# Kernel tuning notes

Hardware: AMD Instinct MI355X
Metric: run time of the kernel (lower is better)

## Reference

```python
import jax, jax.numpy as jnp
import numpy as np

N_E = 1024      # nconcepts (codebook size)
E_DIM = 64      # cdim (codebook vector dim)
BETA = 0.25
LEGACY = True


def setup_inputs() -> dict:
    key = jax.random.key(0)
    k1, k2, k3 = jax.random.split(key, 3)
    z_ = jax.random.normal(k1, (32, 256, 32, 32), jnp.float32)
    # 1x1 conv dis_modulator: 256 -> 64 channels (stored as [out, in])
    conv_w = jax.random.normal(k2, (64, 256), jnp.float32) / np.sqrt(256.0)
    conv_b = jnp.zeros((64,), jnp.float32)
    # embedding.weight.data.uniform_(-1/n_e, 1/n_e)
    emb = jax.random.uniform(k3, (N_E, E_DIM), jnp.float32, -1.0 / N_E, 1.0 / N_E)
    return {"z_": z_, "conv_w": conv_w, "conv_b": conv_b, "emb": emb}


def _forward(z_, conv_w, conv_b, emb):
    sg = jax.lax.stop_gradient
    # dis_modulator: 1x1 conv == per-pixel linear map  (B,Cin,H,W)->(B,Cout,H,W)
    z = jnp.einsum('bchw,oc->bohw', z_, conv_w) + conv_b[None, :, None, None]
    B = z.shape[0]
    # torch .view(-1, e_dim): row-major flatten of (B,C,H,W) into chunks of e_dim
    zf = z.reshape(-1, E_DIM)  # [B*C*H*W/e_dim, e_dim]

    # contrastive term: mean pairwise cosine similarity of codebook rows
    d1 = emb @ emb.T                                  # [n_e, n_e]
    norms = jnp.linalg.norm(emb, axis=1)              # [n_e]
    cosine = d1 / (norms[:, None] * norms[None, :])
    contrastive = jnp.mean(cosine)

    # squared L2 distances: ||z||^2 + ||e||^2 - 2 z.e
    d = (jnp.sum(zf * zf, axis=1, keepdims=True)
         + jnp.sum(emb * emb, axis=1)[None, :]
         - 2.0 * (zf @ emb.T))                        # [N, n_e]
    idx = jnp.argmin(d, axis=1)                       # [N]
    z_q = emb[idx].reshape(z.shape)

    if LEGACY:
        loss = jnp.mean((sg(z_q) - z) ** 2) + BETA * jnp.mean((z_q - sg(z)) ** 2)
    else:
        loss = BETA * jnp.mean((sg(z_q) - z) ** 2) + jnp.mean((z_q - sg(z)) ** 2)
    # hessian_penalty(G, z_, G_z=z): G is an affine 1x1 conv, so the central
    # second difference G(z+x) - 2G(z) + G(z-x) is identically zero -> penalty = 0.
    loss = loss + contrastive

    # straight-through estimator
    z_q_st = z + sg(z_q - z)

    # replicate source exactly: flat zeros(B*n_e) scattered at codebook indices
    sampled = jnp.zeros((B * N_E,), z.dtype).at[idx].set(1.0).reshape(B, N_E)
    min_idx = idx.reshape(B, -1)
    return z_q_st, loss, sampled, min_idx


def reference(z_, conv_w, conv_b, emb):
    z_q, loss, sampled, min_idx = _forward(z_, conv_w, conv_b, emb)
    return z_q, loss, sampled, min_idx
```

## Files before the change

kernel.cpp:

```cpp
#include <hip/hip_runtime.h>

#define BATCH   32
#define CIN     256
#define COUT    64
#define HW      1024
#define NE      1024
#define ED      64
#define NROW    32768
#define ZTOT    2097152

#define OFF_LOSS 2097152
#define OFF_SAMP 2097153
#define OFF_IDX  2129921

#define CXSTR 132
#define CWSTR 68
#define ZSTR  132
#define ESTR  132

__global__ __launch_bounds__(256, 2) void k_pre(const float* __restrict__ x,
                                                const float* __restrict__ w,
                                                const float* __restrict__ bias,
                                                float* __restrict__ z,
                                                const float* __restrict__ emb,
                                                float* __restrict__ out_samp,
                                                float* __restrict__ enorm,
                                                float* __restrict__ cpart,
                                                unsigned int* __restrict__ counter) {
    __shared__ float SH[64 * CXSTR + 64 * CWSTR];
    int bx = blockIdx.x;
    int t  = threadIdx.x;

    if (bx < 128) {
        if (bx == 0 && t == 0) *counter = 0u;
        out_samp[bx * 256 + t] = 0.0f;
        return;
    }
    if (bx < 144) {
        float* invl = SH;
        float* S    = SH + 64;
        int b2 = bx - 128;
        int i0 = b2 * 64;
        if (t < 64) {
            const float* e = emb + (size_t)(i0 + t) * ED;
            float r8[8];
            #pragma unroll
            for (int s = 0; s < 8; s++) { float xx = e[s]; r8[s] = xx * xx; }
            #pragma unroll
            for (int m = 1; m < 8; m++) {
                #pragma unroll
                for (int s = 0; s < 8; s++) { float xx = e[8 * m + s]; r8[s] += xx * xx; }
            }
            float en = ((r8[0] + r8[1]) + (r8[2] + r8[3])) + ((r8[4] + r8[5]) + (r8[6] + r8[7]));
            invl[t] = 1.0f / sqrtf(en);
        }
        __syncthreads();
        int d = t & 63, q = t >> 6;
        float s = 0.0f;
        #pragma unroll
        for (int m = 0; m < 16; m++) {
            int il = q + 4 * m;
            s = fmaf(emb[(size_t)(i0 + il) * ED + d], invl[il], s);
        }
        S[t] = s;
        __syncthreads();
        if (t < 64)
            cpart[b2 * 64 + t] = (S[t] + S[t + 64]) + (S[t + 128] + S[t + 192]);
        return;
    }
    if (bx < 148) {
        int j = (bx - 144) * 256 + t;
        const float* e = emb + (size_t)j * ED;
        float r8[8];
        #pragma unroll
        for (int s = 0; s < 8; s++) { float xx = e[s]; r8[s] = xx * xx; }
        #pragma unroll
        for (int m = 1; m < 8; m++) {
            #pragma unroll
            for (int s = 0; s < 8; s++) { float xx = e[8 * m + s]; r8[s] += xx * xx; }
        }
        enorm[j] = ((r8[0] + r8[1]) + (r8[2] + r8[3])) + ((r8[4] + r8[5]) + (r8[6] + r8[7]));
        return;
    }

    float* Xs = SH;
    float* Ws = SH + 64 * CXSTR;
    int cbx = bx - 148;
    int b   = cbx >> 3;
    int p0  = (cbx & 7) * 128;
    int pg  = t & 15;
    int og  = t >> 4;
    float acc[8][4];
    #pragma unroll
    for (int i = 0; i < 8; i++)
        #pragma unroll
        for (int j = 0; j < 4; j++) acc[i][j] = 0.0f;

    for (int c0 = 0; c0 < CIN; c0 += 64) {
        __syncthreads();
        {
            int u = t & 31, cc = t >> 5;
            #pragma unroll
            for (int m = 0; m < 8; m++) {
                int c = cc + 8 * m;
                float4 v = *(const float4*)&x[(size_t)(b * CIN + c0 + c) * HW + p0 + 4 * u];
                *(float4*)&Xs[c * CXSTR + 4 * u] = v;
            }
            int u2 = t & 15, o2 = t >> 4;
            #pragma unroll
            for (int m = 0; m < 4; m++) {
                int o = o2 + 16 * m;
                float4 v = *(const float4*)&w[o * CIN + c0 + 4 * u2];
                Ws[(4 * u2 + 0) * CWSTR + o] = v.x;
                Ws[(4 * u2 + 1) * CWSTR + o] = v.y;
                Ws[(4 * u2 + 2) * CWSTR + o] = v.z;
                Ws[(4 * u2 + 3) * CWSTR + o] = v.w;
            }
        }
        __syncthreads();
        #pragma unroll 4
        for (int k = 0; k < 64; k++) {
            float4 xa4 = *(const float4*)&Xs[k * CXSTR + 4 * pg];
            float4 xb4 = *(const float4*)&Xs[k * CXSTR + 64 + 4 * pg];
            float4 wv4 = *(const float4*)&Ws[k * CWSTR + 4 * og];
            float xa[8] = {xa4.x, xa4.y, xa4.z, xa4.w, xb4.x, xb4.y, xb4.z, xb4.w};
            float wb[4] = {wv4.x, wv4.y, wv4.z, wv4.w};
            #pragma unroll
            for (int i = 0; i < 8; i++)
                #pragma unroll
                for (int j = 0; j < 4; j++)
                    acc[i][j] = fmaf(xa[i], wb[j], acc[i][j]);
        }
    }
    #pragma unroll
    for (int j = 0; j < 4; j++) {
        int o = 4 * og + j;
        float bv = bias[o];
        float4 lo, hi;
        lo.x = acc[0][j] + bv; lo.y = acc[1][j] + bv;
        lo.z = acc[2][j] + bv; lo.w = acc[3][j] + bv;
        hi.x = acc[4][j] + bv; hi.y = acc[5][j] + bv;
        hi.z = acc[6][j] + bv; hi.w = acc[7][j] + bv;
        *(float4*)&z[(size_t)(b * COUT + o) * HW + p0 + 4 * pg]      = lo;
        *(float4*)&z[(size_t)(b * COUT + o) * HW + p0 + 64 + 4 * pg] = hi;
    }
}

__global__ __launch_bounds__(256, 2) void k_dist(const float* __restrict__ z,
                                                 const float* __restrict__ emb,
                                                 const float* __restrict__ enorm,
                                                 const float* __restrict__ cpart,
                                                 float* __restrict__ out_idx,
                                                 float* __restrict__ out_samp,
                                                 float* __restrict__ out_zq,
                                                 float* __restrict__ ssep,
                                                 float* __restrict__ out_loss,
                                                 unsigned int* __restrict__ counter) {
    __shared__ float zs[64 * ZSTR];
    __shared__ float es[64 * ESTR];
    __shared__ float zn_s[128];
    __shared__ float en_s[128];
    __shared__ float warr[4];
    __shared__ int   lastflag;
    __shared__ float CS;
    float* redd_s = es;
    int*   redj_s = (int*)(es + 2048);
    int*   bj_s   = (int*)(es + 4096);
    int t = threadIdx.x;
    int row0 = blockIdx.x * 128;
    int rg = t & 15;
    int cg = t >> 4;

    {
        int k = t & 63, wv = t >> 6;
        #pragma unroll
        for (int m = 0; m < 8; m++) {
            int v = wv + 4 * m;
            float4 val;
            val.x = z[(size_t)(row0 + 4 * v + 0) * ED + k];
            val.y = z[(size_t)(row0 + 4 * v + 1) * ED + k];
            val.z = z[(size_t)(row0 + 4 * v + 2) * ED + k];
            val.w = z[(size_t)(row0 + 4 * v + 3) * ED + k];
            *(float4*)&zs[k * ZSTR + 4 * v] = val;
        }
    }
    __syncthreads();
    if (t < 128) {
        float r8[8];
        #pragma unroll
        for (int s = 0; s < 8; s++) { float xx = zs[s * ZSTR + t]; r8[s] = xx * xx; }
        #pragma unroll
        for (int m = 1; m < 8; m++) {
            #pragma unroll
            for (int s = 0; s < 8; s++) { float xx = zs[(8 * m + s) * ZSTR + t]; r8[s] += xx * xx; }
        }
        zn_s[t] = ((r8[0] + r8[1]) + (r8[2] + r8[3])) + ((r8[4] + r8[5]) + (r8[6] + r8[7]));
    }

    float bestd[8];
    int   bestj[8];
    #pragma unroll
    for (int i = 0; i < 8; i++) { bestd[i] = __builtin_huge_valf(); bestj[i] = 0; }

    for (int ch = 0; ch < 8; ch++) {
        int c0 = ch * 128;
        __syncthreads();
        {
            int k = t & 63, wv = t >> 6;
            #pragma unroll
            for (int m = 0; m < 8; m++) {
                int v = wv + 4 * m;
                float4 val;
                val.x = emb[(size_t)(c0 + 4 * v + 0) * ED + k];
                val.y = emb[(size_t)(c0 + 4 * v + 1) * ED + k];
                val.z = emb[(size_t)(c0 + 4 * v + 2) * ED + k];
                val.w = emb[(size_t)(c0 + 4 * v + 3) * ED + k];
                *(float4*)&es[k * ESTR + 4 * v] = val;
            }
            if (t < 32) {
                float4 ev4 = *(const float4*)&enorm[c0 + 4 * t];
                *(float4*)&en_s[4 * t] = ev4;
            }
        }
        __syncthreads();

        float acc[8][8];
        #pragma unroll
        for (int i = 0; i < 8; i++)
            #pragma unroll
            for (int j = 0; j < 8; j++) acc[i][j] = 0.0f;

        #pragma unroll 4
        for (int k = 0; k < 64; k++) {
            float4 za = *(const float4*)&zs[k * ZSTR + 4 * rg];
            float4 zb = *(const float4*)&zs[k * ZSTR + 64 + 4 * rg];
            float4 e0 = *(const float4*)&es[k * ESTR + 8 * cg];
            float4 e1 = *(const float4*)&es[k * ESTR + 8 * cg + 4];
            float xa[8] = {za.x, za.y, za.z, za.w, zb.x, zb.y, zb.z, zb.w};
            float eb[8] = {e0.x, e0.y, e0.z, e0.w, e1.x, e1.y, e1.z, e1.w};
            #pragma unroll
            for (int i = 0; i < 8; i++)
                #pragma unroll
                for (int j = 0; j < 8; j++)
                    acc[i][j] = fmaf(xa[i], eb[j], acc[i][j]);
        }

        #pragma unroll
        for (int i = 0; i < 8; i++) {
            int rl = (i < 4) ? (4 * rg + i) : (64 + 4 * rg + (i - 4));
            float zn = zn_s[rl];
            #pragma unroll
            for (int j = 0; j < 8; j++) {
                int cl = 8 * cg + j;
                float A = zn + en_s[cl];
                float D = A - 2.0f * acc[i][j];
                if (D < bestd[i]) { bestd[i] = D; bestj[i] = c0 + cl; }
            }
        }
    }

    __syncthreads();
    #pragma unroll
    for (int i = 0; i < 8; i++) {
        int rl = (i < 4) ? (4 * rg + i) : (64 + 4 * rg + (i - 4));
        redd_s[cg * 128 + rl] = bestd[i];
        redj_s[cg * 128 + rl] = bestj[i];
    }
    __syncthreads();
    if (t < 128) {
        float bd = __builtin_huge_valf();
        int   bj = 0x7fffffff;
        #pragma unroll
        for (int c = 0; c < 16; c++) {
            float dd = redd_s[c * 128 + t];
            int   jj = redj_s[c * 128 + t];
            if (dd < bd || (dd == bd && jj < bj)) { bd = dd; bj = jj; }
        }
        int rowg = row0 + t;
        bj_s[t]       = bj;
        out_idx[rowg] = (float)bj;
        atomicExch(&out_samp[bj], 1.0f);
    }
    __syncthreads();

    {
        int r  = t & 127;
        int kq = t >> 7;
        int bj = bj_s[r];
        const float* er = emb + (size_t)bj * ED + kq * 32;
        float sq = 0.0f;
        #pragma unroll
        for (int m = 0; m < 8; m++) {
            float4 ev = *(const float4*)&er[4 * m];
            int kk = kq * 32 + 4 * m;
            float zv0 = zs[(kk + 0) * ZSTR + r];
            float zv1 = zs[(kk + 1) * ZSTR + r];
            float zv2 = zs[(kk + 2) * ZSTR + r];
            float zv3 = zs[(kk + 3) * ZSTR + r];
            float d0 = ev.x - zv0, d1 = ev.y - zv1, d2 = ev.z - zv2, d3 = ev.w - zv3;
            float4 o4;
            o4.x = zv0 + d0; o4.y = zv1 + d1; o4.z = zv2 + d2; o4.w = zv3 + d3;
            *(float4*)&out_zq[(size_t)(row0 + r) * ED + kk] = o4;
            sq += d0 * d0; sq += d1 * d1; sq += d2 * d2; sq += d3 * d3;
        }
        #pragma unroll
        for (int off = 32; off > 0; off >>= 1) sq += __shfl_down(sq, off, 64);
        if ((t & 63) == 0) warr[t >> 6] = sq;
    }
    __syncthreads();

    if (t == 0) {
        ssep[blockIdx.x] = (warr[0] + warr[1]) + (warr[2] + warr[3]);
        __threadfence();
        unsigned int old = atomicAdd(counter, 1u);
        lastflag = (old == 255u) ? 1 : 0;
    }
    __syncthreads();
    if (lastflag) {
        __threadfence();
        double* SD = (double*)es;
        const volatile float* sv = (const volatile float*)ssep;
        SD[t] = (double)sv[t];
        __syncthreads();
        #pragma unroll
        for (int off = 128; off > 0; off >>= 1) {
            if (t < off) SD[t] += SD[t + off];
            __syncthreads();
        }
        if (t < 64) {
            float v = 0.0f;
            #pragma unroll
            for (int m = 0; m < 16; m++) v += cpart[m * 64 + t];
            float sq = v * v;
            #pragma unroll
            for (int off = 32; off > 0; off >>= 1) sq += __shfl_down(sq, off, 64);
            if (t == 0) CS = sq / (1024.0f * 1024.0f);
        }
        __syncthreads();
        if (t == 0) {
            float m = (float)(SD[0] / (double)ZTOT);
            float loss = m + 0.25f * m;
            out_loss[0] = loss + CS;
        }
    }
}

extern "C" void kernel_launch(void* const* d_in, const int* in_sizes, int n_in,
                              void* d_out, int out_size, void* d_ws, size_t ws_size,
                              hipStream_t stream) {
    (void)in_sizes; (void)n_in; (void)out_size; (void)ws_size;
    const float* z_     = (const float*)d_in[0];
    const float* conv_w = (const float*)d_in[1];
    const float* conv_b = (const float*)d_in[2];
    const float* emb    = (const float*)d_in[3];

    float* out      = (float*)d_out;
    float* out_zq   = out;
    float* out_loss = out + OFF_LOSS;
    float* out_samp = out + OFF_SAMP;
    float* out_idx  = out + OFF_IDX;

    char*  ws       = (char*)d_ws;
    float* wz       = (float*)ws;
    float* enorm    = (float*)(ws + 8388608);
    float* cpart    = (float*)(ws + 8392704);
    float* ssep     = (float*)(ws + 8396800);
    unsigned int* counter = (unsigned int*)(ws + 8397824);

    k_pre  <<<404, 256, 0, stream>>>(z_, conv_w, conv_b, wz, emb, out_samp, enorm, cpart, counter);
    k_dist <<<256, 256, 0, stream>>>(wz, emb, enorm, cpart, out_idx, out_samp, out_zq, ssep, out_loss, counter);
}
```

Baseline: 183.9 us.

## Retile distance kernel to 64-row blocks with row-major smem and k-split codebook chunks

The distance/argmin kernel now handles 64 rows per block instead of 128 and launches 512 blocks, so more of the device's compute units get work. Shared memory switches from a k-major transposed layout to row-major padded rows loaded with float4 and coalesced global reads. Codebook chunks grow to 256 entries, staged in two 32-wide k halves, and each thread computes an 8x8 tile through float4 dot-product loads. This trades more codebook reloads per output row and a wider 32-way cross-thread reduction for better load coalescing and parallelism.

```diff
diff --git a/kernel.cpp b/kernel.cpp
--- a/kernel.cpp
+++ b/kernel.cpp
@@ -15,8 +15,8 @@
 
 #define CXSTR 132
 #define CWSTR 68
-#define ZSTR  132
-#define ESTR  132
+#define ZROWS 68
+#define EROWS 36
 
 __global__ __launch_bounds__(256, 2) void k_pre(const float* __restrict__ x,
                                                 const float* __restrict__ w,
@@ -156,10 +156,10 @@
                                                  float* __restrict__ ssep,
                                                  float* __restrict__ out_loss,
                                                  unsigned int* __restrict__ counter) {
-    __shared__ float zs[64 * ZSTR];
-    __shared__ float es[64 * ESTR];
-    __shared__ float zn_s[128];
-    __shared__ float en_s[128];
+    __shared__ float zs[64 * ZROWS];
+    __shared__ float es[256 * EROWS];
+    __shared__ float zn_s[64];
+    __shared__ float en_s[256];
     __shared__ float warr[4];
     __shared__ int   lastflag;
     __shared__ float CS;
@@ -167,32 +167,29 @@
     int*   redj_s = (int*)(es + 2048);
     int*   bj_s   = (int*)(es + 4096);
     int t = threadIdx.x;
-    int row0 = blockIdx.x * 128;
-    int rg = t & 15;
-    int cg = t >> 4;
+    int row0 = blockIdx.x * 64;
+    int rg = t >> 5;
+    int cg = t & 31;
 
     {
-        int k = t & 63, wv = t >> 6;
-        #pragma unroll
-        for (int m = 0; m < 8; m++) {
-            int v = wv + 4 * m;
-            float4 val;
-            val.x = z[(size_t)(row0 + 4 * v + 0) * ED + k];
-            val.y = z[(size_t)(row0 + 4 * v + 1) * ED + k];
-            val.z = z[(size_t)(row0 + 4 * v + 2) * ED + k];
-            val.w = z[(size_t)(row0 + 4 * v + 3) * ED + k];
-            *(float4*)&zs[k * ZSTR + 4 * v] = val;
-        }
-    }
-    __syncthreads();
-    if (t < 128) {
+        int k4 = t & 15, rr = t >> 4;
+        #pragma unroll
+        for (int m = 0; m < 4; m++) {
+            int r = rr + 16 * m;
+            float4 v = *(const float4*)&z[(size_t)(row0 + r) * ED + 4 * k4];
+            *(float4*)&zs[r * ZROWS + 4 * k4] = v;
+        }
+    }
+    __syncthreads();
+    if (t < 64) {
+        const float* zr = &zs[t * ZROWS];
         float r8[8];
         #pragma unroll
-        for (int s = 0; s < 8; s++) { float xx = zs[s * ZSTR + t]; r8[s] = xx * xx; }
+        for (int s = 0; s < 8; s++) { float xx = zr[s]; r8[s] = xx * xx; }
         #pragma unroll
         for (int m = 1; m < 8; m++) {
             #pragma unroll
-            for (int s = 0; s < 8; s++) { float xx = zs[(8 * m + s) * ZSTR + t]; r8[s] += xx * xx; }
+            for (int s = 0; s < 8; s++) { float xx = zr[8 * m + s]; r8[s] += xx * xx; }
         }
         zn_s[t] = ((r8[0] + r8[1]) + (r8[2] + r8[3])) + ((r8[4] + r8[5]) + (r8[6] + r8[7]));
     }
@@ -202,56 +199,59 @@
     #pragma unroll
     for (int i = 0; i < 8; i++) { bestd[i] = __builtin_huge_valf(); bestj[i] = 0; }
 
-    for (int ch = 0; ch < 8; ch++) {
-        int c0 = ch * 128;
-        __syncthreads();
-        {
-            int k = t & 63, wv = t >> 6;
-            #pragma unroll
-            for (int m = 0; m < 8; m++) {
-                int v = wv + 4 * m;
-                float4 val;
-                val.x = emb[(size_t)(c0 + 4 * v + 0) * ED + k];
-                val.y = emb[(size_t)(c0 + 4 * v + 1) * ED + k];
-                val.z = emb[(size_t)(c0 + 4 * v + 2) * ED + k];
-                val.w = emb[(size_t)(c0 + 4 * v + 3) * ED + k];
-                *(float4*)&es[k * ESTR + 4 * v] = val;
-            }
-            if (t < 32) {
-                float4 ev4 = *(const float4*)&enorm[c0 + 4 * t];
-                *(float4*)&en_s[4 * t] = ev4;
-            }
-        }
-        __syncthreads();
-
+    for (int ch = 0; ch < 4; ch++) {
+        int c0 = ch * 256;
         float acc[8][8];
         #pragma unroll
         for (int i = 0; i < 8; i++)
             #pragma unroll
             for (int j = 0; j < 8; j++) acc[i][j] = 0.0f;
 
-        #pragma unroll 4
-        for (int k = 0; k < 64; k++) {
-            float4 za = *(const float4*)&zs[k * ZSTR + 4 * rg];
-            float4 zb = *(const float4*)&zs[k * ZSTR + 64 + 4 * rg];
-            float4 e0 = *(const float4*)&es[k * ESTR + 8 * cg];
-            float4 e1 = *(const float4*)&es[k * ESTR + 8 * cg + 4];
-            float xa[8] = {za.x, za.y, za.z, za.w, zb.x, zb.y, zb.z, zb.w};
-            float eb[8] = {e0.x, e0.y, e0.z, e0.w, e1.x, e1.y, e1.z, e1.w};
-            #pragma unroll
-            for (int i = 0; i < 8; i++)
+        for (int kh = 0; kh < 2; kh++) {
+            __syncthreads();
+            {
+                int k4 = t & 7, cc = t >> 3;
+                #pragma unroll
+                for (int m = 0; m < 8; m++) {
+                    int c = cc + 32 * m;
+                    float4 v = *(const float4*)&emb[(size_t)(c0 + c) * ED + kh * 32 + 4 * k4];
+                    *(float4*)&es[c * EROWS + 4 * k4] = v;
+                }
+                if (kh == 0 && t < 64) {
+                    float4 ev = *(const float4*)&enorm[c0 + 4 * t];
+                    *(float4*)&en_s[4 * t] = ev;
+                }
+            }
+            __syncthreads();
+
+            int kb = kh * 32;
+            #pragma unroll 2
+            for (int ks = 0; ks < 8; ks++) {
+                float4 za[8], eb[8];
+                #pragma unroll
+                for (int i = 0; i < 8; i++)
+                    za[i] = *(const float4*)&zs[(rg + 8 * i) * ZROWS + kb + 4 * ks];
                 #pragma unroll
                 for (int j = 0; j < 8; j++)
-                    acc[i][j] = fmaf(xa[i], eb[j], acc[i][j]);
+                    eb[j] = *(const float4*)&es[(cg + 32 * j) * EROWS + 4 * ks];
+                #pragma unroll
+                for (int i = 0; i < 8; i++)
+                    #pragma unroll
+                    for (int j = 0; j < 8; j++) {
+                        acc[i][j] = fmaf(za[i].x, eb[j].x, acc[i][j]);
+                        acc[i][j] = fmaf(za[i].y, eb[j].y, acc[i][j]);
+                        acc[i][j] = fmaf(za[i].z, eb[j].z, acc[i][j]);
+                        acc[i][j] = fmaf(za[i].w, eb[j].w, acc[i][j]);
+                    }
+            }
         }
 
         #pragma unroll
         for (int i = 0; i < 8; i++) {
-            int rl = (i < 4) ? (4 * rg + i) : (64 + 4 * rg + (i - 4));
-            float zn = zn_s[rl];
+            float zn = zn_s[rg + 8 * i];
             #pragma unroll
             for (int j = 0; j < 8; j++) {
-                int cl = 8 * cg + j;
+                int cl = cg + 32 * j;
                 float A = zn + en_s[cl];
                 float D = A - 2.0f * acc[i][j];
                 if (D < bestd[i]) { bestd[i] = D; bestj[i] = c0 + cl; }
@@ -262,18 +262,18 @@
     __syncthreads();
     #pragma unroll
     for (int i = 0; i < 8; i++) {
-        int rl = (i < 4) ? (4 * rg + i) : (64 + 4 * rg + (i - 4));
-        redd_s[cg * 128 + rl] = bestd[i];
-        redj_s[cg * 128 + rl] = bestj[i];
-    }
-    __syncthreads();
-    if (t < 128) {
+        int rl = rg + 8 * i;
+        redd_s[cg * 64 + rl] = bestd[i];
+        redj_s[cg * 64 + rl] = bestj[i];
+    }
+    __syncthreads();
+    if (t < 64) {
         float bd = __builtin_huge_valf();
         int   bj = 0x7fffffff;
         #pragma unroll
-        for (int c = 0; c < 16; c++) {
-            float dd = redd_s[c * 128 + t];
-            int   jj = redj_s[c * 128 + t];
+        for (int c = 0; c < 32; c++) {
+            float dd = redd_s[c * 64 + t];
+            int   jj = redj_s[c * 64 + t];
             if (dd < bd || (dd == bd && jj < bj)) { bd = dd; bj = jj; }
         }
         int rowg = row0 + t;
@@ -284,23 +284,20 @@
     __syncthreads();
 
     {
-        int r  = t & 127;
-        int kq = t >> 7;
+        int r  = t & 63;
+        int kq = t >> 6;
         int bj = bj_s[r];
-        const float* er = emb + (size_t)bj * ED + kq * 32;
+        const float* er = emb + (size_t)bj * ED + kq * 16;
+        const float* zr = &zs[r * ZROWS + kq * 16];
         float sq = 0.0f;
         #pragma unroll
-        for (int m = 0; m < 8; m++) {
+        for (int m = 0; m < 4; m++) {
             float4 ev = *(const float4*)&er[4 * m];
-            int kk = kq * 32 + 4 * m;
-            float zv0 = zs[(kk + 0) * ZSTR + r];
-            float zv1 = zs[(kk + 1) * ZSTR + r];
-            float zv2 = zs[(kk + 2) * ZSTR + r];
-            float zv3 = zs[(kk + 3) * ZSTR + r];
-            float d0 = ev.x - zv0, d1 = ev.y - zv1, d2 = ev.z - zv2, d3 = ev.w - zv3;
+            float4 zv = *(const float4*)&zr[4 * m];
+            float d0 = ev.x - zv.x, d1 = ev.y - zv.y, d2 = ev.z - zv.z, d3 = ev.w - zv.w;
             float4 o4;
-            o4.x = zv0 + d0; o4.y = zv1 + d1; o4.z = zv2 + d2; o4.w = zv3 + d3;
-            *(float4*)&out_zq[(size_t)(row0 + r) * ED + kk] = o4;
+            o4.x = zv.x + d0; o4.y = zv.y + d1; o4.z = zv.z + d2; o4.w = zv.w + d3;
+            *(float4*)&out_zq[(size_t)(row0 + r) * ED + kq * 16 + 4 * m] = o4;
             sq += d0 * d0; sq += d1 * d1; sq += d2 * d2; sq += d3 * d3;
         }
         #pragma unroll
@@ -313,14 +310,14 @@
         ssep[blockIdx.x] = (warr[0] + warr[1]) + (warr[2] + warr[3]);
         __threadfence();
         unsigned int old = atomicAdd(counter, 1u);
-        lastflag = (old == 255u) ? 1 : 0;
+        lastflag = (old == 511u) ? 1 : 0;
     }
     __syncthreads();
     if (lastflag) {
         __threadfence();
         double* SD = (double*)es;
         const volatile float* sv = (const volatile float*)ssep;
-        SD[t] = (double)sv[t];
+        SD[t] = (double)sv[t] + (double)sv[t + 256];
         __syncthreads();
         #pragma unroll
         for (int off = 128; off > 0; off >>= 1) {
@@ -365,8 +362,8 @@
     float* enorm    = (float*)(ws + 8388608);
     float* cpart    = (float*)(ws + 8392704);
     float* ssep     = (float*)(ws + 8396800);
-    unsigned int* counter = (unsigned int*)(ws + 8397824);
+    unsigned int* counter = (unsigned int*)(ws + 8398848);
 
     k_pre  <<<404, 256, 0, stream>>>(z_, conv_w, conv_b, wz, emb, out_samp, enorm, cpart, counter);
-    k_dist <<<256, 256, 0, stream>>>(wz, emb, enorm, cpart, out_idx, out_samp, out_zq, ssep, out_loss, counter);
+    k_dist <<<512, 256, 0, stream>>>(wz, emb, enorm, cpart, out_idx, out_samp, out_zq, ssep, out_loss, counter);
 }
```

After: 185.3 us. About the same (+0.8%).

## Fuse 1x1 conv into distance kernel and keep z tile in shared memory

Applied to the files above, without the earlier changes.

The conv GEMM moves into the distance/argmin kernel, so each block computes its 64 flattened rows of z directly into shared memory. This removes the write of the 8 MB z intermediate to global memory and its read back. It relies on the fact that a 64-pixel strip of the conv output for one batch maps to 64 rows of the flattened view at stride 16. The tile shrinks from 128 to 64 rows and the grid grows to 512 blocks, which means more codebook reloads per row and smaller per-thread register tiles.

```diff
diff --git a/kernel.cpp b/kernel.cpp
--- a/kernel.cpp
+++ b/kernel.cpp
@@ -6,39 +6,32 @@
 #define HW      1024
 #define NE      1024
 #define ED      64
-#define NROW    32768
 #define ZTOT    2097152
 
 #define OFF_LOSS 2097152
 #define OFF_SAMP 2097153
 #define OFF_IDX  2129921
 
-#define CXSTR 132
-#define CWSTR 68
-#define ZSTR  132
-#define ESTR  132
-
-__global__ __launch_bounds__(256, 2) void k_pre(const float* __restrict__ x,
-                                                const float* __restrict__ w,
-                                                const float* __restrict__ bias,
-                                                float* __restrict__ z,
-                                                const float* __restrict__ emb,
-                                                float* __restrict__ out_samp,
-                                                float* __restrict__ enorm,
-                                                float* __restrict__ cpart,
-                                                unsigned int* __restrict__ counter) {
-    __shared__ float SH[64 * CXSTR + 64 * CWSTR];
+#define CSTR 66
+#define ESTR 132
+#define ZSTR 68
+
+__global__ __launch_bounds__(256) void k_con(const float* __restrict__ emb,
+                                             float* __restrict__ out_samp,
+                                             float* __restrict__ enorm,
+                                             float* __restrict__ cpart,
+                                             unsigned int* __restrict__ counter) {
+    __shared__ float SHc[320];
     int bx = blockIdx.x;
     int t  = threadIdx.x;
-
     if (bx < 128) {
         if (bx == 0 && t == 0) *counter = 0u;
         out_samp[bx * 256 + t] = 0.0f;
         return;
     }
     if (bx < 144) {
-        float* invl = SH;
-        float* S    = SH + 64;
+        float* invl = SHc;
+        float* S    = SHc + 64;
         int b2 = bx - 128;
         int i0 = b2 * 64;
         if (t < 64) {
@@ -68,7 +61,7 @@
             cpart[b2 * 64 + t] = (S[t] + S[t + 64]) + (S[t + 128] + S[t + 192]);
         return;
     }
-    if (bx < 148) {
+    {
         int j = (bx - 144) * 256 + t;
         const float* e = emb + (size_t)j * ED;
         float r8[8];
@@ -80,127 +73,116 @@
             for (int s = 0; s < 8; s++) { float xx = e[8 * m + s]; r8[s] += xx * xx; }
         }
         enorm[j] = ((r8[0] + r8[1]) + (r8[2] + r8[3])) + ((r8[4] + r8[5]) + (r8[6] + r8[7]));
-        return;
-    }
-
-    float* Xs = SH;
-    float* Ws = SH + 64 * CXSTR;
-    int cbx = bx - 148;
-    int b   = cbx >> 3;
-    int p0  = (cbx & 7) * 128;
-    int pg  = t & 15;
-    int og  = t >> 4;
-    float acc[8][4];
-    #pragma unroll
-    for (int i = 0; i < 8; i++)
-        #pragma unroll
-        for (int j = 0; j < 4; j++) acc[i][j] = 0.0f;
-
-    for (int c0 = 0; c0 < CIN; c0 += 64) {
-        __syncthreads();
-        {
-            int u = t & 31, cc = t >> 5;
-            #pragma unroll
-            for (int m = 0; m < 8; m++) {
-                int c = cc + 8 * m;
-                float4 v = *(const float4*)&x[(size_t)(b * CIN + c0 + c) * HW + p0 + 4 * u];
-                *(float4*)&Xs[c * CXSTR + 4 * u] = v;
-            }
-            int u2 = t & 15, o2 = t >> 4;
-            #pragma unroll
-            for (int m = 0; m < 4; m++) {
-                int o = o2 + 16 * m;
-                float4 v = *(const float4*)&w[o * CIN + c0 + 4 * u2];
-                Ws[(4 * u2 + 0) * CWSTR + o] = v.x;
-                Ws[(4 * u2 + 1) * CWSTR + o] = v.y;
-                Ws[(4 * u2 + 2) * CWSTR + o] = v.z;
-                Ws[(4 * u2 + 3) * CWSTR + o] = v.w;
-            }
-        }
-        __syncthreads();
-        #pragma unroll 4
-        for (int k = 0; k < 64; k++) {
-            float4 xa4 = *(const float4*)&Xs[k * CXSTR + 4 * pg];
-            float4 xb4 = *(const float4*)&Xs[k * CXSTR + 64 + 4 * pg];
-            float4 wv4 = *(const float4*)&Ws[k * CWSTR + 4 * og];
-            float xa[8] = {xa4.x, xa4.y, xa4.z, xa4.w, xb4.x, xb4.y, xb4.z, xb4.w};
-            float wb[4] = {wv4.x, wv4.y, wv4.z, wv4.w};
-            #pragma unroll
-            for (int i = 0; i < 8; i++)
-                #pragma unroll
-                for (int j = 0; j < 4; j++)
-                    acc[i][j] = fmaf(xa[i], wb[j], acc[i][j]);
-        }
-    }
-    #pragma unroll
-    for (int j = 0; j < 4; j++) {
-        int o = 4 * og + j;
-        float bv = bias[o];
-        float4 lo, hi;
-        lo.x = acc[0][j] + bv; lo.y = acc[1][j] + bv;
-        lo.z = acc[2][j] + bv; lo.w = acc[3][j] + bv;
-        hi.x = acc[4][j] + bv; hi.y = acc[5][j] + bv;
-        hi.z = acc[6][j] + bv; hi.w = acc[7][j] + bv;
-        *(float4*)&z[(size_t)(b * COUT + o) * HW + p0 + 4 * pg]      = lo;
-        *(float4*)&z[(size_t)(b * COUT + o) * HW + p0 + 64 + 4 * pg] = hi;
     }
 }
 
-__global__ __launch_bounds__(256, 2) void k_dist(const float* __restrict__ z,
-                                                 const float* __restrict__ emb,
-                                                 const float* __restrict__ enorm,
-                                                 const float* __restrict__ cpart,
-                                                 float* __restrict__ out_idx,
-                                                 float* __restrict__ out_samp,
-                                                 float* __restrict__ out_zq,
-                                                 float* __restrict__ ssep,
-                                                 float* __restrict__ out_loss,
-                                                 unsigned int* __restrict__ counter) {
+__global__ __launch_bounds__(256, 2) void k_fused(const float* __restrict__ x,
+                                                  const float* __restrict__ w,
+                                                  const float* __restrict__ bias,
+                                                  const float* __restrict__ emb,
+                                                  const float* __restrict__ enorm,
+                                                  const float* __restrict__ cpart,
+                                                  float* __restrict__ out_idx,
+                                                  float* __restrict__ out_samp,
+                                                  float* __restrict__ out_zq,
+                                                  float* __restrict__ ssep,
+                                                  float* __restrict__ out_loss,
+                                                  unsigned int* __restrict__ counter) {
+    __shared__ float SH[64 * CSTR * 2];
     __shared__ float zs[64 * ZSTR];
-    __shared__ float es[64 * ESTR];
-    __shared__ float zn_s[128];
+    __shared__ float zn_s[64];
     __shared__ float en_s[128];
     __shared__ float warr[4];
+    __shared__ int   bj_s[64];
     __shared__ int   lastflag;
     __shared__ float CS;
-    float* redd_s = es;
-    int*   redj_s = (int*)(es + 2048);
-    int*   bj_s   = (int*)(es + 4096);
-    int t = threadIdx.x;
-    int row0 = blockIdx.x * 128;
+    __shared__ double SD[256];
+    float* redd_s = SH;
+    int*   redj_s = (int*)(SH + 1024);
+
+    int t  = threadIdx.x;
+    int bx = blockIdx.x;
+    int b   = bx >> 4;
+    int p16 = bx & 15;
+    int p0  = p16 * 64;
+
+    {
+        float* Xs = SH;
+        float* Ws = SH + 64 * CSTR;
+        int pg = t & 15;
+        int og = t >> 4;
+        float acc[4][4];
+        #pragma unroll
+        for (int i = 0; i < 4; i++)
+            #pragma unroll
+            for (int j = 0; j < 4; j++) acc[i][j] = 0.0f;
+
+        for (int c0 = 0; c0 < CIN; c0 += 64) {
+            __syncthreads();
+            {
+                int u = t & 15, cg2 = t >> 4;
+                #pragma unroll
+                for (int m = 0; m < 4; m++) {
+                    int c = cg2 + 16 * m;
+                    float4 v = *(const float4*)&x[(size_t)(b * CIN + c0 + c) * HW + p0 + 4 * u];
+                    *(float4*)&Xs[c * CSTR + 4 * u] = v;
+                }
+                #pragma unroll
+                for (int m = 0; m < 4; m++) {
+                    int o = cg2 + 16 * m;
+                    float4 v = *(const float4*)&w[o * CIN + c0 + 4 * u];
+                    Ws[(4 * u + 0) * CSTR + o] = v.x;
+                    Ws[(4 * u + 1) * CSTR + o] = v.y;
+                    Ws[(4 * u + 2) * CSTR + o] = v.z;
+                    Ws[(4 * u + 3) * CSTR + o] = v.w;
+                }
+            }
+            __syncthreads();
+            #pragma unroll 8
+            for (int k = 0; k < 64; k++) {
+                float4 xv = *(const float4*)&Xs[k * CSTR + 4 * pg];
+                float4 wv = *(const float4*)&Ws[k * CSTR + 4 * og];
+                float xa[4] = {xv.x, xv.y, xv.z, xv.w};
+                float wb[4] = {wv.x, wv.y, wv.z, wv.w};
+                #pragma unroll
+                for (int i = 0; i < 4; i++)
+                    #pragma unroll
+                    for (int j = 0; j < 4; j++)
+                        acc[i][j] = fmaf(xa[i], wb[j], acc[i][j]);
+            }
+        }
+        float4 bv4 = *(const float4*)&bias[4 * og];
+        #pragma unroll
+        for (int i = 0; i < 4; i++) {
+            float4 w4;
+            w4.x = acc[i][0] + bv4.x;
+            w4.y = acc[i][1] + bv4.y;
+            w4.z = acc[i][2] + bv4.z;
+            w4.w = acc[i][3] + bv4.w;
+            *(float4*)&zs[(4 * pg + i) * ZSTR + 4 * og] = w4;
+        }
+    }
+    __syncthreads();
+
+    if (t < 64) {
+        float r8[8];
+        #pragma unroll
+        for (int s = 0; s < 8; s++) { float xx = zs[s * ZSTR + t]; r8[s] = xx * xx; }
+        #pragma unroll
+        for (int m = 1; m < 8; m++) {
+            #pragma unroll
+            for (int s = 0; s < 8; s++) { float xx = zs[(8 * m + s) * ZSTR + t]; r8[s] += xx * xx; }
+        }
+        zn_s[t] = ((r8[0] + r8[1]) + (r8[2] + r8[3])) + ((r8[4] + r8[5]) + (r8[6] + r8[7]));
+    }
+
+    float* es = SH;
     int rg = t & 15;
     int cg = t >> 4;
-
-    {
-        int k = t & 63, wv = t >> 6;
-        #pragma unroll
-        for (int m = 0; m < 8; m++) {
-            int v = wv + 4 * m;
-            float4 val;
-            val.x = z[(size_t)(row0 + 4 * v + 0) * ED + k];
-            val.y = z[(size_t)(row0 + 4 * v + 1) * ED + k];
-            val.z = z[(size_t)(row0 + 4 * v + 2) * ED + k];
-            val.w = z[(size_t)(row0 + 4 * v + 3) * ED + k];
-            *(float4*)&zs[k * ZSTR + 4 * v] = val;
-        }
-    }
-    __syncthreads();
-    if (t < 128) {
-        float r8[8];
-        #pragma unroll
-        for (int s = 0; s < 8; s++) { float xx = zs[s * ZSTR + t]; r8[s] = xx * xx; }
-        #pragma unroll
-        for (int m = 1; m < 8; m++) {
-            #pragma unroll
-            for (int s = 0; s < 8; s++) { float xx = zs[(8 * m + s) * ZSTR + t]; r8[s] += xx * xx; }
-        }
-        zn_s[t] = ((r8[0] + r8[1]) + (r8[2] + r8[3])) + ((r8[4] + r8[5]) + (r8[6] + r8[7]));
-    }
-
-    float bestd[8];
-    int   bestj[8];
+    float bestd[4];
+    int   bestj[4];
     #pragma unroll
-    for (int i = 0; i < 8; i++) { bestd[i] = __builtin_huge_valf(); bestj[i] = 0; }
+    for (int i = 0; i < 4; i++) { bestd[i] = __builtin_huge_valf(); bestj[i] = 0; }
 
     for (int ch = 0; ch < 8; ch++) {
         int c0 = ch * 128;
@@ -224,31 +206,29 @@
         }
         __syncthreads();
 
-        float acc[8][8];
-        #pragma unroll
-        for (int i = 0; i < 8; i++)
+        float acc[4][8];
+        #pragma unroll
+        for (int i = 0; i < 4; i++)
             #pragma unroll
             for (int j = 0; j < 8; j++) acc[i][j] = 0.0f;
 
-        #pragma unroll 4
+        #pragma unroll 8
         for (int k = 0; k < 64; k++) {
-            float4 za = *(const float4*)&zs[k * ZSTR + 4 * rg];
-            float4 zb = *(const float4*)&zs[k * ZSTR + 64 + 4 * rg];
+            float4 xv = *(const float4*)&zs[k * ZSTR + 4 * rg];
             float4 e0 = *(const float4*)&es[k * ESTR + 8 * cg];
             float4 e1 = *(const float4*)&es[k * ESTR + 8 * cg + 4];
-            float xa[8] = {za.x, za.y, za.z, za.w, zb.x, zb.y, zb.z, zb.w};
+            float xa[4] = {xv.x, xv.y, xv.z, xv.w};
             float eb[8] = {e0.x, e0.y, e0.z, e0.w, e1.x, e1.y, e1.z, e1.w};
             #pragma unroll
-            for (int i = 0; i < 8; i++)
+            for (int i = 0; i < 4; i++)
                 #pragma unroll
                 for (int j = 0; j < 8; j++)
                     acc[i][j] = fmaf(xa[i], eb[j], acc[i][j]);
         }
 
         #pragma unroll
-        for (int i = 0; i < 8; i++) {
-            int rl = (i < 4) ? (4 * rg + i) : (64 + 4 * rg + (i - 4));
-            float zn = zn_s[rl];
+        for (int i = 0; i < 4; i++) {
+            float zn = zn_s[4 * rg + i];
             #pragma unroll
             for (int j = 0; j < 8; j++) {
                 int cl = 8 * cg + j;
@@ -261,22 +241,21 @@
 
     __syncthreads();
     #pragma unroll
-    for (int i = 0; i < 8; i++) {
-        int rl = (i < 4) ? (4 * rg + i) : (64 + 4 * rg + (i - 4));
-        redd_s[cg * 128 + rl] = bestd[i];
-        redj_s[cg * 128 + rl] = bestj[i];
-    }
-    __syncthreads();
-    if (t < 128) {
+    for (int i = 0; i < 4; i++) {
+        redd_s[cg * 64 + 4 * rg + i] = bestd[i];
+        redj_s[cg * 64 + 4 * rg + i] = bestj[i];
+    }
+    __syncthreads();
+    if (t < 64) {
         float bd = __builtin_huge_valf();
         int   bj = 0x7fffffff;
         #pragma unroll
         for (int c = 0; c < 16; c++) {
-            float dd = redd_s[c * 128 + t];
-            int   jj = redj_s[c * 128 + t];
+            float dd = redd_s[c * 64 + t];
+            int   jj = redj_s[c * 64 + t];
             if (dd < bd || (dd == bd && jj < bj)) { bd = dd; bj = jj; }
         }
-        int rowg = row0 + t;
+        int rowg = b * 1024 + t * 16 + p16;
         bj_s[t]       = bj;
         out_idx[rowg] = (float)bj;
         atomicExch(&out_samp[bj], 1.0f);
@@ -284,15 +263,16 @@
     __syncthreads();
 
     {
-        int r  = t & 127;
-        int kq = t >> 7;
+        int r  = t & 63;
+        int kq = t >> 6;
         int bj = bj_s[r];
-        const float* er = emb + (size_t)bj * ED + kq * 32;
+        size_t n = (size_t)(b * 1024 + r * 16 + p16);
+        const float* er = emb + (size_t)bj * ED + kq * 16;
         float sq = 0.0f;
         #pragma unroll
-        for (int m = 0; m < 8; m++) {
+        for (int m = 0; m < 4; m++) {
             float4 ev = *(const float4*)&er[4 * m];
-            int kk = kq * 32 + 4 * m;
+            int kk = kq * 16 + 4 * m;
             float zv0 = zs[(kk + 0) * ZSTR + r];
             float zv1 = zs[(kk + 1) * ZSTR + r];
             float zv2 = zs[(kk + 2) * ZSTR + r];
@@ -300,7 +280,7 @@
             float d0 = ev.x - zv0, d1 = ev.y - zv1, d2 = ev.z - zv2, d3 = ev.w - zv3;
             float4 o4;
             o4.x = zv0 + d0; o4.y = zv1 + d1; o4.z = zv2 + d2; o4.w = zv3 + d3;
-            *(float4*)&out_zq[(size_t)(row0 + r) * ED + kk] = o4;
+            *(float4*)&out_zq[n * ED + kk] = o4;
             sq += d0 * d0; sq += d1 * d1; sq += d2 * d2; sq += d3 * d3;
         }
         #pragma unroll
@@ -310,17 +290,16 @@
     __syncthreads();
 
     if (t == 0) {
-        ssep[blockIdx.x] = (warr[0] + warr[1]) + (warr[2] + warr[3]);
+        ssep[bx] = (warr[0] + warr[1]) + (warr[2] + warr[3]);
         __threadfence();
         unsigned int old = atomicAdd(counter, 1u);
-        lastflag = (old == 255u) ? 1 : 0;
+        lastflag = (old == 511u) ? 1 : 0;
     }
     __syncthreads();
     if (lastflag) {
         __threadfence();
-        double* SD = (double*)es;
         const volatile float* sv = (const volatile float*)ssep;
-        SD[t] = (double)sv[t];
+        SD[t] = (double)sv[t] + (double)sv[t + 256];
         __syncthreads();
         #pragma unroll
         for (int off = 128; off > 0; off >>= 1) {
@@ -360,13 +339,13 @@
     float* out_samp = out + OFF_SAMP;
     float* out_idx  = out + OFF_IDX;
 
-    char*  ws       = (char*)d_ws;
-    float* wz       = (float*)ws;
-    float* enorm    = (float*)(ws + 8388608);
-    float* cpart    = (float*)(ws + 8392704);
-    float* ssep     = (float*)(ws + 8396800);
-    unsigned int* counter = (unsigned int*)(ws + 8397824);
-
-    k_pre  <<<404, 256, 0, stream>>>(z_, conv_w, conv_b, wz, emb, out_samp, enorm, cpart, counter);
-    k_dist <<<256, 256, 0, stream>>>(wz, emb, enorm, cpart, out_idx, out_samp, out_zq, ssep, out_loss, counter);
+    float* ws    = (float*)d_ws;
+    float* enorm = ws;
+    float* cpart = ws + 1024;
+    float* ssep  = ws + 2048;
+    unsigned int* counter = (unsigned int*)(ws + 2560);
+
+    k_con  <<<148, 256, 0, stream>>>(emb, out_samp, enorm, cpart, counter);
+    k_fused<<<512, 256, 0, stream>>>(z_, conv_w, conv_b, emb, enorm, cpart,
+                                     out_idx, out_samp, out_zq, ssep, out_loss, counter);
 }
```

Result: slower. 218.7 us (+18.9%).
